# Optimization experiments

Hardware: AMD Instinct MI355X
Metric: run time of the kernel (lower is better)

## Reference

```python
import jax, jax.numpy as jnp
import numpy as np

N, E, T, D, A = 16384, 65536, 2048, 64, 6


def _w(k, shape, fan_in):
    return jax.random.normal(k, shape, jnp.float32) / np.sqrt(fan_in)


def setup_inputs() -> dict:
    key = jax.random.key(0)
    ks = jax.random.split(key, 20)
    inp = {}
    inp["x"] = jax.random.normal(ks[0], (N, 3), jnp.float32)
    inp["edge_attr"] = jax.random.normal(ks[1], (E, 7), jnp.float32)
    inp["edge_index"] = jax.random.randint(ks[2], (2, E), 0, N)
    inp["nonring"] = jax.random.randint(ks[3], (T, 4), 0, N)
    inp["hx"] = jnp.zeros((1, D), jnp.float32)
    inp["cx"] = jnp.zeros((1, D), jnp.float32)
    inp["W_lin0"] = _w(ks[4], (D, 3), 3); inp["b_lin0"] = jnp.zeros((D,), jnp.float32)
    inp["W_e1"] = _w(ks[5], (128, 7), 7); inp["b_e1"] = jnp.zeros((128,), jnp.float32)
    inp["W_e2"] = _w(ks[6], (D * D, 128), 128); inp["b_e2"] = jnp.zeros((D * D,), jnp.float32)
    inp["conv_root"] = _w(ks[7], (D, D), D); inp["conv_bias"] = jnp.zeros((D,), jnp.float32)
    inp["gru_Wih"] = _w(ks[8], (3 * D, D), D); inp["gru_Whh"] = _w(ks[9], (3 * D, D), D)
    inp["gru_bih"] = jnp.zeros((3 * D,), jnp.float32); inp["gru_bhh"] = jnp.zeros((3 * D,), jnp.float32)
    inp["s2s_Wih"] = _w(ks[10], (4 * D, 2 * D), 2 * D); inp["s2s_Whh"] = _w(ks[11], (4 * D, D), D)
    inp["s2s_bih"] = jnp.zeros((4 * D,), jnp.float32); inp["s2s_bhh"] = jnp.zeros((4 * D,), jnp.float32)
    inp["mem_Wih"] = _w(ks[12], (4 * D, 2 * D), 2 * D); inp["mem_Whh"] = _w(ks[13], (4 * D, D), D)
    inp["mem_bih"] = jnp.zeros((4 * D,), jnp.float32); inp["mem_bhh"] = jnp.zeros((4 * D,), jnp.float32)
    inp["W_lin1"] = _w(ks[14], (D, 5 * D), 5 * D); inp["b_lin1"] = jnp.zeros((D,), jnp.float32)
    inp["W_lin2"] = _w(ks[15], (A, D), D); inp["b_lin2"] = jnp.zeros((A,), jnp.float32)
    inp["W_lin3"] = _w(ks[16], (1, 3 * D), 3 * D); inp["b_lin3"] = jnp.zeros((1,), jnp.float32)
    return inp


def _lstm_cell(xin, h, c, Wih, Whh, bih, bhh):
    g = xin @ Wih.T + bih + h @ Whh.T + bhh
    i, f, gg, o = jnp.split(g, 4, axis=-1)  # torch gate order i,f,g,o
    c = jax.nn.sigmoid(f) * c + jax.nn.sigmoid(i) * jnp.tanh(gg)
    h = jax.nn.sigmoid(o) * jnp.tanh(c)
    return h, c


def _gru_cell(xin, h, Wih, Whh, bih, bhh):
    gi = xin @ Wih.T + bih
    gh = h @ Whh.T + bhh
    ir, iz, inn = jnp.split(gi, 3, axis=-1)  # torch gate order r,z,n
    hr, hz, hn = jnp.split(gh, 3, axis=-1)
    r = jax.nn.sigmoid(ir + hr)
    z = jax.nn.sigmoid(iz + hz)
    n = jnp.tanh(inn + r * hn)
    return (1.0 - z) * n + z * h


def reference(x, edge_attr, edge_index, nonring, hx, cx,
              W_lin0, b_lin0, W_e1, b_e1, W_e2, b_e2, conv_root, conv_bias,
              gru_Wih, gru_Whh, gru_bih, gru_bhh,
              s2s_Wih, s2s_Whh, s2s_bih, s2s_bhh,
              mem_Wih, mem_Whh, mem_bih, mem_bhh,
              W_lin1, b_lin1, W_lin2, b_lin2, W_lin3, b_lin3):
    src, tgt = edge_index[0], edge_index[1]
    out = jax.nn.relu(x @ W_lin0.T + b_lin0)  # [N, D]
    h = out  # GRU hidden (nodes as batch)
    # edge-conditioned dim x dim matrices (NNConv edge MLP)
    ew = jax.nn.relu(edge_attr @ W_e1.T + b_e1)
    ew = (ew @ W_e2.T + b_e2).reshape(E, D, D)  # [E, D, D]
    cnt = jnp.maximum(jax.ops.segment_sum(jnp.ones((E,), out.dtype), tgt, num_segments=N), 1.0)
    for _ in range(3):
        msg = jnp.einsum('ed,edf->ef', out[src], ew)  # per-edge small matmul
        aggr = jax.ops.segment_sum(msg, tgt, num_segments=N) / cnt[:, None]  # scatter-mean
        m = jax.nn.relu(aggr + out @ conv_root + conv_bias)  # NNConv root + bias, then relu
        h = _gru_cell(m, h, gru_Wih, gru_Whh, gru_bih, gru_bhh)
        out = h
    # Set2Set pooling (single graph, B=1), processing_steps=3
    hs = jnp.zeros((1, D), out.dtype)
    cs = jnp.zeros((1, D), out.dtype)
    q_star = jnp.zeros((1, 2 * D), out.dtype)
    for _ in range(3):
        hs, cs = _lstm_cell(q_star, hs, cs, s2s_Wih, s2s_Whh, s2s_bih, s2s_bhh)
        a = jax.nn.softmax(out @ hs[0])  # [N]
        r = (a[:, None] * out).sum(0, keepdims=True)  # [1, D]
        q_star = jnp.concatenate([hs, r], axis=1)
    pool = q_star  # [1, 2D]
    lstm_out, cx_new = _lstm_cell(pool, hx, cx, mem_Wih, mem_Whh, mem_bih, mem_bhh)
    hx_new = lstm_out
    # torsion head: index_select -> view(4*D, -1) -> permute(1,0)
    sel = out[nonring.reshape(-1)]  # [4T, D]
    tfeat = sel.reshape(4 * D, -1).T  # [T, 4D], faithful to torch view semantics
    rep = jnp.repeat(lstm_out.reshape(-1), T).reshape(T, D)  # torch repeat_interleave + view
    pf = jnp.concatenate([tfeat, rep], axis=1)  # [T, 5D]
    logits = jax.nn.relu(pf @ W_lin1.T + b_lin1) @ W_lin2.T + b_lin2  # [T, A]
    v = jnp.concatenate([pool, lstm_out], axis=1) @ W_lin3.T + b_lin3  # [1, 1]
    return logits, v, hx_new, cx_new
```

## Files before the change

kernel.cpp:

```cpp
#include <hip/hip_runtime.h>

#define cN 16384
#define cE 65536
#define cT 2048
#define CAP 88

typedef __attribute__((ext_vector_type(8))) short short8;
typedef __attribute__((ext_vector_type(4))) float f32x4;
typedef __attribute__((ext_vector_type(4))) unsigned u32x4;

__device__ __forceinline__ short f2bf(float f){
  unsigned u = __float_as_uint(f);
  u = (u + 0x7FFFu + ((u >> 16) & 1u)) >> 16;
  return (short)u;
}
__device__ __forceinline__ float bf2f(short s){
  return __uint_as_float(((unsigned)(unsigned short)s) << 16);
}
__device__ __forceinline__ unsigned cvtpk(float lo, float hi){
  unsigned r;
  asm("v_cvt_pk_bf16_f32 %0, %1, %2" : "=v"(r) : "v"(lo), "v"(hi));
  return r;
}
__device__ __forceinline__ float sigm(float x){ return 1.f / (1.f + __expf(-x)); }
__device__ __forceinline__ float wred(float v){
  v += __shfl_xor(v, 32); v += __shfl_xor(v, 16); v += __shfl_xor(v, 8);
  v += __shfl_xor(v, 4);  v += __shfl_xor(v, 2);  v += __shfl_xor(v, 1);
  return v;
}
__device__ __forceinline__ float wredmax(float v){
  v = fmaxf(v, __shfl_xor(v, 32)); v = fmaxf(v, __shfl_xor(v, 16));
  v = fmaxf(v, __shfl_xor(v, 8));  v = fmaxf(v, __shfl_xor(v, 4));
  v = fmaxf(v, __shfl_xor(v, 2));  v = fmaxf(v, __shfl_xor(v, 1));
  return v;
}

#define B_L0   4096
#define B_H1   20480
#define B_W2   22528
#define B_B2   22544
#define B_WP   22656
#define B_DEG  22912
__global__ __launch_bounds__(256) void k_setup(
    const float* __restrict__ x, const float* __restrict__ Wl0, const float* __restrict__ bl0,
    float* __restrict__ out,
    const float* __restrict__ ea, const float* __restrict__ We1, const float* __restrict__ be1,
    unsigned* __restrict__ h1p,
    const float* __restrict__ W2, short* __restrict__ w2f,
    const float* __restrict__ b2, short* __restrict__ b2f,
    const float* __restrict__ convW, const float* __restrict__ gWih,
    const float* __restrict__ gWhh, short* __restrict__ wpk,
    const int* __restrict__ ei, int* __restrict__ deg)
{
  int b = blockIdx.x, tid = threadIdx.x;
  if (b < B_L0){
    int i = b * 256 + tid;
    int n = i >> 6, f = i & 63;
    float acc = bl0[f] + x[n*3]*Wl0[f*3] + x[n*3+1]*Wl0[f*3+1] + x[n*3+2]*Wl0[f*3+2];
    out[i] = fmaxf(acc, 0.f);
  } else if (b < B_H1){
    int i = (b - B_L0) * 256 + tid;
    int e = i >> 6, k = i & 63;
    const float* a  = ea + e * 7;
    const float* w0 = We1 + k * 7;
    const float* w1 = We1 + (k + 64) * 7;
    float a0 = be1[k], a1 = be1[k + 64];
    #pragma unroll
    for (int c = 0; c < 7; c++){ float av = a[c]; a0 += av * w0[c]; a1 += av * w1[c]; }
    unsigned lo = (unsigned short)f2bf(fmaxf(a0, 0.f));
    unsigned hi = (unsigned short)f2bf(fmaxf(a1, 0.f));
    h1p[i] = lo | (hi << 16);
  } else if (b < B_W2){
    int o = (b - B_H1) * 256 + tid;
    int j = o & 7, l = (o >> 3) & 63, ks = (o >> 9) & 31, c = (o >> 14) & 7, fb = (o >> 17) & 3;
    int f = fb * 16 + (l & 15);
    int d = c * 8 + j;
    int k = ks * 4 + ((l >> 4) & 3);
    w2f[o] = f2bf(W2[(d * 64 + f) * 128 + k]);
  } else if (b < B_B2){
    int o = (b - B_W2) * 256 + tid;
    int j = o & 7, l = (o >> 3) & 63, ks2 = (o >> 9) & 1, fb = (o >> 10) & 3;
    int d = ks2 * 32 + ((l >> 4) & 3) * 8 + j;
    int f = fb * 16 + (l & 15);
    b2f[o] = f2bf(b2[d * 64 + f]);
  } else if (b < B_WP){
    int o = (b - B_B2) * 256 + tid;
    int j = o & 7, l = (o >> 3) & 63, kc = (o >> 9) & 1, cb = o >> 10;
    int k = kc * 32 + ((l >> 4) & 3) * 8 + j;
    int c16 = l & 15;
    float v;
    if (cb < 4)       v = convW[k * 64 + cb * 16 + c16];
    else if (cb < 16) v = gWih[((cb - 4) * 16 + c16) * 64 + k];
    else              v = gWhh[((cb - 16) * 16 + c16) * 64 + k];
    wpk[o] = f2bf(v);
  } else {
    int e = (b - B_WP) * 256 + tid;
    atomicAdd(&deg[ei[cE + e]], 1);
  }
}

__global__ __launch_bounds__(1024) void k_scan(const int* __restrict__ deg,
    int* __restrict__ rowp, int* __restrict__ cur, float* __restrict__ cnt)
{
  __shared__ int part[1024];
  int tid = threadIdx.x;
  int base = tid * 16;
  int loc[16]; int s = 0;
  #pragma unroll
  for (int i = 0; i < 16; i++){ loc[i] = s; s += deg[base + i]; }
  part[tid] = s;
  __syncthreads();
  for (int off = 1; off < 1024; off <<= 1){
    int v = (tid >= off) ? part[tid - off] : 0;
    __syncthreads();
    part[tid] += v;
    __syncthreads();
  }
  int inc = part[tid];
  int eb = inc - s;
  #pragma unroll
  for (int i = 0; i < 16; i++){
    int rv = eb + loc[i];
    rowp[base + i] = rv;
    cur[base + i] = rv;
    int dv = deg[base + i];
    cnt[base + i] = (float)(dv > 0 ? dv : 1);
  }
  if (tid == 1023) rowp[16384] = inc;
}

__global__ __launch_bounds__(256) void k_scatter(const int* __restrict__ ei,
    int* __restrict__ cur, int* __restrict__ esrc, int* __restrict__ eidx)
{
  int e = blockIdx.x * 256 + threadIdx.x;
  int t = ei[cE + e];
  int pos = atomicAdd(&cur[t], 1);
  esrc[pos] = ei[e];
  eidx[pos] = e;
}

__global__ __launch_bounds__(256, 2) void k_sagg(const float* __restrict__ outR,
    float* __restrict__ outW,
    const unsigned* __restrict__ h1p, const short* __restrict__ w2f,
    const short* __restrict__ b2f, const short* __restrict__ wpk,
    const float* __restrict__ convB, const float* __restrict__ bih,
    const float* __restrict__ bhh, const float* __restrict__ cnt,
    const int* __restrict__ rowp, const int* __restrict__ esrc,
    const int* __restrict__ eidx)
{
  __shared__ __align__(16) short S[16][1040];
  __shared__ __align__(16) unsigned h1i[CAP][64];
  __shared__ __align__(16) float outsf[CAP][64];
  __shared__ __align__(16) short osb[16][72];
  int tid = threadIdx.x, w = tid >> 6, lane = tid & 63;
  int t0 = blockIdx.x * 16;

  int ebase = rowp[t0];
  int eend  = rowp[t0 + 16];
  int ecnt  = eend - ebase;
  bool fits = (ecnt <= CAP);
  int scnt  = fits ? ecnt : CAP;
  for (int i = w; i < scnt; i += 4){
    int eid = eidx[ebase + i];
    int src = esrc[ebase + i];
    h1i[i][lane] = h1p[(size_t)eid * 64 + lane];
    outsf[i][lane] = outR[(size_t)src * 64 + lane];
  }
  int toff[4], tcnt[4];
  #pragma unroll
  for (int g = 0; g < 4; g++){
    int t = t0 + w * 4 + g;
    int a = rowp[t], b = rowp[t + 1];
    toff[g] = a - ebase; tcnt[g] = b - a;
  }
  short8 breg[32];
  {
    const short* bb0 = w2f + ((size_t)(w * 8) * 32) * 512 + lane * 8;
    #pragma unroll
    for (int ks = 0; ks < 32; ++ks)
      breg[ks] = *(const short8*)(bb0 + (size_t)ks * 512);
  }
  __syncthreads();

  #pragma unroll
  for (int g = 0; g < 4; g++){
    int ti = w * 4 + g;
    float os = 0.f;
    int tf = toff[g], tc = tcnt[g];
    for (int p = 0; p < tc; p++){
      int slot = tf + p;
      if (slot < CAP) os += outsf[slot][lane];
      else            os += outR[(size_t)esrc[ebase + slot] * 64 + lane];
    }
    osb[ti][lane] = (short)cvtpk(os, os);
  }

  f32x4 acc[4] = {{0,0,0,0},{0,0,0,0},{0,0,0,0},{0,0,0,0}};
  int arow = lane & 15, kg = lane >> 4;
  for (int c = 0; c < 8; ++c){
    #pragma unroll
    for (int g = 0; g < 4; ++g){
      int ti = w * 4 + g;
      float a0[8], a1[8];
      #pragma unroll
      for (int d = 0; d < 8; d++){ a0[d] = 0.f; a1[d] = 0.f; }
      int tc = tcnt[g], tf = toff[g];
      if (fits){
        #pragma unroll 2
        for (int p = 0; p < tc; ++p){
          int slot = tf + p;
          unsigned u = h1i[slot][lane];
          float h1a = __uint_as_float(u << 16);
          float h1b = __uint_as_float(u & 0xFFFF0000u);
          f32x4 o0 = *(const f32x4*)&outsf[slot][c * 8];
          f32x4 o1 = *(const f32x4*)&outsf[slot][c * 8 + 4];
          a0[0] = fmaf(o0[0], h1a, a0[0]); a1[0] = fmaf(o0[0], h1b, a1[0]);
          a0[1] = fmaf(o0[1], h1a, a0[1]); a1[1] = fmaf(o0[1], h1b, a1[1]);
          a0[2] = fmaf(o0[2], h1a, a0[2]); a1[2] = fmaf(o0[2], h1b, a1[2]);
          a0[3] = fmaf(o0[3], h1a, a0[3]); a1[3] = fmaf(o0[3], h1b, a1[3]);
          a0[4] = fmaf(o1[0], h1a, a0[4]); a1[4] = fmaf(o1[0], h1b, a1[4]);
          a0[5] = fmaf(o1[1], h1a, a0[5]); a1[5] = fmaf(o1[1], h1b, a1[5]);
          a0[6] = fmaf(o1[2], h1a, a0[6]); a1[6] = fmaf(o1[2], h1b, a1[6]);
          a0[7] = fmaf(o1[3], h1a, a0[7]); a1[7] = fmaf(o1[3], h1b, a1[7]);
        }
      } else {
        for (int p = 0; p < tc; ++p){
          int slot = tf + p;
          if (slot < CAP){
            unsigned u = h1i[slot][lane];
            float h1a = __uint_as_float(u << 16);
            float h1b = __uint_as_float(u & 0xFFFF0000u);
            f32x4 o0 = *(const f32x4*)&outsf[slot][c * 8];
            f32x4 o1 = *(const f32x4*)&outsf[slot][c * 8 + 4];
            #pragma unroll
            for (int d = 0; d < 4; d++){
              a0[d] = fmaf(o0[d], h1a, a0[d]); a1[d] = fmaf(o0[d], h1b, a1[d]);
              a0[4+d] = fmaf(o1[d], h1a, a0[4+d]); a1[4+d] = fmaf(o1[d], h1b, a1[4+d]);
            }
          } else {
            int eid = eidx[ebase + slot];
            int src = esrc[ebase + slot];
            unsigned u = h1p[(size_t)eid * 64 + lane];
            float h1a = __uint_as_float(u << 16);
            float h1b = __uint_as_float(u & 0xFFFF0000u);
            #pragma unroll
            for (int d = 0; d < 8; d++){
              float o = outR[(size_t)src * 64 + c * 8 + d];
              a0[d] = fmaf(o, h1a, a0[d]); a1[d] = fmaf(o, h1b, a1[d]);
            }
          }
        }
      }
      u32x4 p0, p1;
      p0[0] = cvtpk(a0[0], a0[1]); p0[1] = cvtpk(a0[2], a0[3]);
      p0[2] = cvtpk(a0[4], a0[5]); p0[3] = cvtpk(a0[6], a0[7]);
      p1[0] = cvtpk(a1[0], a1[1]); p1[1] = cvtpk(a1[2], a1[3]);
      p1[2] = cvtpk(a1[4], a1[5]); p1[3] = cvtpk(a1[6], a1[7]);
      *(u32x4*)&S[ti][lane * 8]       = p0;
      *(u32x4*)&S[ti][512 + lane * 8] = p1;
    }
    __syncthreads();
    const short* bbn = w2f + ((size_t)(w * 8 + c + 1) * 32) * 512 + lane * 8;
    bool more = (c < 7);
    #pragma unroll
    for (int ks8 = 0; ks8 < 8; ++ks8){
      #pragma unroll
      for (int j = 0; j < 4; ++j){
        int ks = ks8 * 4 + j;
        short8 afr = *(const short8*)&S[arow][ks * 32 + kg * 8];
        acc[j] = __builtin_amdgcn_mfma_f32_16x16x32_bf16(afr, breg[ks], acc[j], 0, 0, 0);
        if (more) breg[ks] = *(const short8*)(bbn + (size_t)ks * 512);
      }
    }
    __syncthreads();
  }
  #pragma unroll
  for (int ks2 = 0; ks2 < 2; ++ks2){
    short8 osf = *(const short8*)&osb[arow][ks2 * 32 + kg * 8];
    short8 bfr = *(const short8*)(b2f + ((size_t)((w * 2 + ks2) * 64 + lane)) * 8);
    acc[ks2] = __builtin_amdgcn_mfma_f32_16x16x32_bf16(osf, bfr, acc[ks2], 0, 0, 0);
  }
  f32x4 accT;
  #pragma unroll
  for (int q = 0; q < 4; q++)
    accT[q] = (acc[0][q] + acc[1][q]) + (acc[2][q] + acc[3][q]);

  int fcol = w * 16 + arow;
  int trow = kg * 4;
  short* tA  = (short*)&h1i[0][0];
  short* mAp = tA + 16 * 72;
  for (int i = tid; i < 512; i += 256){
    int r = i >> 5, c2 = (i & 31) * 2;
    float2 v = *(const float2*)&outR[(size_t)(t0 + r) * 64 + c2];
    *(unsigned*)&tA[r * 72 + c2] = cvtpk(v.x, v.y);
  }
  __syncthreads();
  const short8* WF = (const short8*)wpk;
  short8 aof0 = *(const short8*)&tA[arow * 72 + kg * 8];
  short8 aof1 = *(const short8*)&tA[arow * 72 + 32 + kg * 8];
  f32x4 cz = {0.f, 0.f, 0.f, 0.f};
  f32x4 cva0 = __builtin_amdgcn_mfma_f32_16x16x32_bf16(aof0, WF[(w * 2 + 0) * 64 + lane], cz, 0, 0, 0);
  f32x4 cva1 = __builtin_amdgcn_mfma_f32_16x16x32_bf16(aof1, WF[(w * 2 + 1) * 64 + lane], cz, 0, 0, 0);
  float cb_ = convB[fcol];
  #pragma unroll
  for (int q = 0; q < 4; q++){
    int node = t0 + trow + q;
    float icq = 1.0f / fmaxf(cnt[node], 1.0f);
    float m = fmaxf(accT[q] * icq + cva0[q] + cva1[q] + cb_, 0.f);
    mAp[(trow + q) * 72 + fcol] = f2bf(m);
  }
  __syncthreads();
  short8 amf0 = *(const short8*)&mAp[arow * 72 + kg * 8];
  short8 amf1 = *(const short8*)&mAp[arow * 72 + 32 + kg * 8];
  f32x4 gir = {0,0,0,0}, giz = {0,0,0,0}, gin = {0,0,0,0};
  f32x4 ghr = {0,0,0,0}, ghz = {0,0,0,0}, ghn = {0,0,0,0};
  gir = __builtin_amdgcn_mfma_f32_16x16x32_bf16(amf0, WF[((4  + w) * 2 + 0) * 64 + lane], gir, 0, 0, 0);
  gir = __builtin_amdgcn_mfma_f32_16x16x32_bf16(amf1, WF[((4  + w) * 2 + 1) * 64 + lane], gir, 0, 0, 0);
  giz = __builtin_amdgcn_mfma_f32_16x16x32_bf16(amf0, WF[((8  + w) * 2 + 0) * 64 + lane], giz, 0, 0, 0);
  giz = __builtin_amdgcn_mfma_f32_16x16x32_bf16(amf1, WF[((8  + w) * 2 + 1) * 64 + lane], giz, 0, 0, 0);
  gin = __builtin_amdgcn_mfma_f32_16x16x32_bf16(amf0, WF[((12 + w) * 2 + 0) * 64 + lane], gin, 0, 0, 0);
  gin = __builtin_amdgcn_mfma_f32_16x16x32_bf16(amf1, WF[((12 + w) * 2 + 1) * 64 + lane], gin, 0, 0, 0);
  ghr = __builtin_amdgcn_mfma_f32_16x16x32_bf16(aof0, WF[((16 + w) * 2 + 0) * 64 + lane], ghr, 0, 0, 0);
  ghr = __builtin_amdgcn_mfma_f32_16x16x32_bf16(aof1, WF[((16 + w) * 2 + 1) * 64 + lane], ghr, 0, 0, 0);
  ghz = __builtin_amdgcn_mfma_f32_16x16x32_bf16(aof0, WF[((20 + w) * 2 + 0) * 64 + lane], ghz, 0, 0, 0);
  ghz = __builtin_amdgcn_mfma_f32_16x16x32_bf16(aof1, WF[((20 + w) * 2 + 1) * 64 + lane], ghz, 0, 0, 0);
  ghn = __builtin_amdgcn_mfma_f32_16x16x32_bf16(aof0, WF[((24 + w) * 2 + 0) * 64 + lane], ghn, 0, 0, 0);
  ghn = __builtin_amdgcn_mfma_f32_16x16x32_bf16(aof1, WF[((24 + w) * 2 + 1) * 64 + lane], ghn, 0, 0, 0);
  float bir = bih[fcol], biz = bih[64 + fcol], bin_ = bih[128 + fcol];
  float bhr = bhh[fcol], bhz = bhh[64 + fcol], bhn = bhh[128 + fcol];
  #pragma unroll
  for (int q = 0; q < 4; q++){
    size_t node = (size_t)(t0 + trow + q);
    float rr = sigm(gir[q] + bir + ghr[q] + bhr);
    float zz = sigm(giz[q] + biz + ghz[q] + bhz);
    float nn = tanhf(gin[q] + bin_ + rr * (ghn[q] + bhn));
    float o = outR[node * 64 + fcol];
    outW[node * 64 + fcol] = (1.f - zz) * nn + zz * o;
  }
}

__global__ __launch_bounds__(256) void k_dotsF(const float* __restrict__ out,
    const float* __restrict__ Wih, const float* __restrict__ Whh,
    const float* __restrict__ bih, const float* __restrict__ bhh,
    float* __restrict__ scal,
    const float* __restrict__ rbI, const float* __restrict__ bmI, const float* __restrict__ esI,
    float* __restrict__ rbO, float* __restrict__ bmO, float* __restrict__ esO, int st)
{
  __shared__ float q[128];
  __shared__ float hsL[64];
  __shared__ float gsh[4][64];
  __shared__ float hsh[64];
  __shared__ float smax[4];
  __shared__ float otile[64][64];
  __shared__ float sarr[64];
  __shared__ float ebuf[64];
  __shared__ float rpart[4][64];
  __shared__ float redA[4], redB[4];
  const float* pg = scal + st * 256;
  float* pn = scal + (st + 1) * 256;
  int tid = threadIdx.x, gg = tid >> 6, lane = tid & 63;
  if (st > 0){
    float bm = bmI[tid];
    float m = wredmax(bm);
    if (lane == 0) redA[gg] = m;
    __syncthreads();
    float gmax = fmaxf(fmaxf(redA[0], redA[1]), fmaxf(redA[2], redA[3]));
    float ep = wred(__expf(bm - gmax) * esI[tid]);
    if (lane == 0) redB[gg] = ep;
    float racc = 0.f;
    for (int i = 0; i < 64; i++){
      int b = gg * 64 + i;
      racc += __expf(bmI[b] - gmax) * rbI[b * 64 + lane];
    }
    rpart[gg][lane] = racc;
    __syncthreads();
    if (gg == 0){
      float esum = redB[0] + redB[1] + redB[2] + redB[3];
      float r = rpart[0][lane] + rpart[1][lane] + rpart[2][lane] + rpart[3][lane];
      q[64 + lane] = r / esum;
    }
  } else if (gg == 0) q[64 + lane] = 0.f;
  if (gg == 0){
    float hs = (st == 0) ? 0.f : pg[lane];
    q[lane] = hs; hsL[lane] = hs;
  }
  __syncthreads();
  float2 fq = *(const float2*)&q[2 * lane];
  float hv0 = hsL[lane];
  #pragma unroll 4
  for (int o = 0; o < 64; o++){
    int row = gg * 64 + o;
    float2 wv = *(const float2*)&Wih[(size_t)row * 128 + 2 * lane];
    float s = wv.x * fq.x + wv.y * fq.y + Whh[(size_t)row * 64 + lane] * hv0;
    s = wred(s);
    if (lane == 0) gsh[gg][o] = s;
  }
  __syncthreads();
  if (gg == 0){
    float gi = gsh[0][lane] + bih[lane]       + bhh[lane];
    float gf = gsh[1][lane] + bih[64 + lane]  + bhh[64 + lane];
    float gv = gsh[2][lane] + bih[128 + lane] + bhh[128 + lane];
    float go = gsh[3][lane] + bih[192 + lane] + bhh[192 + lane];
    float cs = (st == 0) ? 0.f : pg[64 + lane];
    float cn = sigm(gf) * cs + sigm(gi) * tanhf(gv);
    float hn = sigm(go) * tanhf(cn);
    hsh[lane] = hn;
    if (blockIdx.x == 0){ pn[lane] = hn; pn[64 + lane] = cn; }
  }
  __syncthreads();
  int nbase = blockIdx.x * 64 + gg * 16;
  float hv = hsh[lane];
  float wmax = -3.4e38f;
  #pragma unroll 4
  for (int i = 0; i < 16; i++){
    float v = out[(size_t)(nbase + i) * 64 + lane];
    otile[gg * 16 + i][lane] = v;
    float p = wred(v * hv);
    if (lane == 0) sarr[gg * 16 + i] = p;
    wmax = fmaxf(wmax, p);
  }
  if (lane == 0) smax[gg] = wmax;
  __syncthreads();
  float bm = fmaxf(fmaxf(smax[0], smax[1]), fmaxf(smax[2], smax[3]));
  if (tid < 64) ebuf[tid] = __expf(sarr[tid] - bm);
  __syncthreads();
  float racc = 0.f;
  #pragma unroll 4
  for (int i = 0; i < 16; i++)
    racc += ebuf[gg * 16 + i] * otile[gg * 16 + i][lane];
  rpart[gg][lane] = racc;
  __syncthreads();
  if (gg == 0){
    float r = rpart[0][lane] + rpart[1][lane] + rpart[2][lane] + rpart[3][lane];
    rbO[blockIdx.x * 64 + lane] = r;
  } else if (gg == 1){
    float es = wred(ebuf[lane]);
    if (lane == 0) esO[blockIdx.x] = es;
  } else if (gg == 2 && lane == 0) bmO[blockIdx.x] = bm;
}

__global__ __launch_bounds__(256) void k_smFin(
    const float* __restrict__ rbI, const float* __restrict__ bmI, const float* __restrict__ esI,
    const float* __restrict__ Wih, const float* __restrict__ Whh,
    const float* __restrict__ bih, const float* __restrict__ bhh,
    const float* __restrict__ hx, const float* __restrict__ cx,
    const float* __restrict__ W3, const float* __restrict__ b3,
    float* __restrict__ scal, float* __restrict__ dout)
{
  __shared__ float redA[4], redB[4];
  __shared__ float rpart[4][64];
  __shared__ float pool[128];
  __shared__ float hxs[64];
  __shared__ float gsh[4][64];
  __shared__ float lob[64];
  int tid = threadIdx.x, wid = tid >> 6, lane = tid & 63;
  float bm = bmI[tid];
  float m = wredmax(bm);
  if (lane == 0) redA[wid] = m;
  __syncthreads();
  float gmax = fmaxf(fmaxf(redA[0], redA[1]), fmaxf(redA[2], redA[3]));
  float ep = wred(__expf(bm - gmax) * esI[tid]);
  if (lane == 0) redB[wid] = ep;
  float racc = 0.f;
  for (int i = 0; i < 64; i++){
    int b = wid * 64 + i;
    racc += __expf(bmI[b] - gmax) * rbI[b * 64 + lane];
  }
  rpart[wid][lane] = racc;
  __syncthreads();
  if (wid == 0){
    float esum = redB[0] + redB[1] + redB[2] + redB[3];
    float r = rpart[0][lane] + rpart[1][lane] + rpart[2][lane] + rpart[3][lane];
    pool[lane] = scal[3 * 256 + lane];
    pool[64 + lane] = r / esum;
    hxs[lane] = hx[lane];
  }
  __syncthreads();
  float2 fq = *(const float2*)&pool[2 * lane];
  float hv = hxs[lane];
  #pragma unroll 4
  for (int o = 0; o < 64; o++){
    int row = wid * 64 + o;
    float2 wv = *(const float2*)&Wih[(size_t)row * 128 + 2 * lane];
    float s = wv.x * fq.x + wv.y * fq.y + Whh[(size_t)row * 64 + lane] * hv;
    s = wred(s);
    if (lane == 0) gsh[wid][o] = s;
  }
  __syncthreads();
  if (wid == 0){
    float gi = gsh[0][lane] + bih[lane]       + bhh[lane];
    float gf = gsh[1][lane] + bih[64 + lane]  + bhh[64 + lane];
    float gv = gsh[2][lane] + bih[128 + lane] + bhh[128 + lane];
    float go = gsh[3][lane] + bih[192 + lane] + bhh[192 + lane];
    float cn = sigm(gf) * cx[lane] + sigm(gi) * tanhf(gv);
    float hn = sigm(go) * tanhf(cn);
    dout[12289 + lane] = hn;
    dout[12353 + lane] = cn;
    scal[1024 + lane] = hn;
    lob[lane] = hn;
  }
  __syncthreads();
  if (wid == 0){
    float a = pool[lane] * W3[lane] + pool[64 + lane] * W3[64 + lane]
            + lob[lane] * W3[128 + lane];
    a = wred(a);
    if (lane == 0) dout[12288] = a + b3[0];
  }
}

__global__ __launch_bounds__(256) void k_head(const float* __restrict__ out,
    const int* __restrict__ nr, const float* __restrict__ scal,
    const float* __restrict__ W1, const float* __restrict__ b1,
    const float* __restrict__ W2, const float* __restrict__ b2,
    float* __restrict__ dout)
{
  __shared__ float pf[4][320];
  __shared__ float hb[4][64];
  int tid = threadIdx.x, wid = tid >> 6, lane = tid & 63;
  int t = blockIdx.x * 4 + wid;
  float lo = scal[1024 + (t >> 5)];
  #pragma unroll
  for (int rep = 0; rep < 4; rep++){
    int j = rep * 64 + lane;
    int idx = nr[j * 32 + (t >> 6)];
    pf[wid][j] = out[idx * 64 + (t & 63)];
  }
  pf[wid][256 + lane] = lo;
  __syncthreads();
  float acc = b1[lane];
  const float* w = W1 + lane * 320;
  #pragma unroll 4
  for (int j = 0; j < 320; j++) acc += pf[wid][j] * w[j];
  hb[wid][lane] = fmaxf(acc, 0.f);
  __syncthreads();
  if (lane < 6){
    float a2 = b2[lane];
    const float* w2 = W2 + lane * 64;
    #pragma unroll 4
    for (int f = 0; f < 64; f++) a2 += hb[wid][f] * w2[f];
    dout[t * 6 + lane] = a2;
  }
}

extern "C" void kernel_launch(void* const* d_in, const int* in_sizes, int n_in,
                              void* d_out, int out_size, void* d_ws, size_t ws_size,
                              hipStream_t stream)
{
  const float* x         = (const float*)d_in[0];
  const float* edge_attr = (const float*)d_in[1];
  const int*   ei        = (const int*)d_in[2];
  const int*   nonring   = (const int*)d_in[3];
  const float* hx        = (const float*)d_in[4];
  const float* cx        = (const float*)d_in[5];
  const float* W_lin0 = (const float*)d_in[6];  const float* b_lin0 = (const float*)d_in[7];
  const float* W_e1   = (const float*)d_in[8];  const float* b_e1   = (const float*)d_in[9];
  const float* W_e2   = (const float*)d_in[10]; const float* b_e2   = (const float*)d_in[11];
  const float* convW  = (const float*)d_in[12]; const float* convB  = (const float*)d_in[13];
  const float* gWih   = (const float*)d_in[14]; const float* gWhh   = (const float*)d_in[15];
  const float* gbih   = (const float*)d_in[16]; const float* gbhh   = (const float*)d_in[17];
  const float* sWih   = (const float*)d_in[18]; const float* sWhh   = (const float*)d_in[19];
  const float* sbih   = (const float*)d_in[20]; const float* sbhh   = (const float*)d_in[21];
  const float* mWih   = (const float*)d_in[22]; const float* mWhh   = (const float*)d_in[23];
  const float* mbih   = (const float*)d_in[24]; const float* mbhh   = (const float*)d_in[25];
  const float* W_lin1 = (const float*)d_in[26]; const float* b_lin1 = (const float*)d_in[27];
  const float* W_lin2 = (const float*)d_in[28]; const float* b_lin2 = (const float*)d_in[29];
  const float* W_lin3 = (const float*)d_in[30]; const float* b_lin3 = (const float*)d_in[31];
  float* dout = (float*)d_out;

  char* w = (char*)d_ws;
  float* outb = (float*)w;  w += (size_t)cN * 64 * 4;
  float* outb2= (float*)w;  w += (size_t)cN * 64 * 4;
  unsigned* h1p = (unsigned*)w;  w += (size_t)cE * 64 * 4;
  short* w2f  = (short*)w;  w += (size_t)64 * 8192 * 2;
  short* b2f  = (short*)w;  w += 4096 * 2;
  short* wpk  = (short*)w;  w += 28672 * 2;
  float* cntb = (float*)w;  w += cN * 4;
  float* rbufA= (float*)w;  w += 256 * 64 * 4;
  float* rbufB= (float*)w;  w += 256 * 64 * 4;
  float* bmA  = (float*)w;  w += 256 * 4;
  float* bmB  = (float*)w;  w += 256 * 4;
  float* esA  = (float*)w;  w += 256 * 4;
  float* esB  = (float*)w;  w += 256 * 4;
  float* scal = (float*)w;  w += 1088 * 4;
  int* deg  = (int*)w;  w += cN * 4;
  int* cur  = (int*)w;  w += cN * 4;
  int* rowp = (int*)w;  w += (cN + 1) * 4 + 60;
  int* esrc = (int*)w;  w += cE * 4;
  int* eidx = (int*)w;  w += cE * 4;

  hipMemsetAsync(deg, 0, cN * 4, stream);

  k_setup<<<B_DEG, 256, 0, stream>>>(x, W_lin0, b_lin0, outb,
      edge_attr, W_e1, b_e1, h1p, W_e2, w2f, b_e2, b2f,
      convW, gWih, gWhh, wpk, ei, deg);
  k_scan<<<1, 1024, 0, stream>>>(deg, rowp, cur, cntb);
  k_scatter<<<cE / 256, 256, 0, stream>>>(ei, cur, esrc, eidx);

  k_sagg<<<cN / 16, 256, 0, stream>>>(outb,  outb2, h1p, w2f, b2f, wpk, convB,
      gbih, gbhh, cntb, rowp, esrc, eidx);
  k_sagg<<<cN / 16, 256, 0, stream>>>(outb2, outb,  h1p, w2f, b2f, wpk, convB,
      gbih, gbhh, cntb, rowp, esrc, eidx);
  k_sagg<<<cN / 16, 256, 0, stream>>>(outb,  outb2, h1p, w2f, b2f, wpk, convB,
      gbih, gbhh, cntb, rowp, esrc, eidx);

  k_dotsF<<<cN / 64, 256, 0, stream>>>(outb2, sWih, sWhh, sbih, sbhh, scal,
      rbufA, bmA, esA, rbufA, bmA, esA, 0);
  k_dotsF<<<cN / 64, 256, 0, stream>>>(outb2, sWih, sWhh, sbih, sbhh, scal,
      rbufA, bmA, esA, rbufB, bmB, esB, 1);
  k_dotsF<<<cN / 64, 256, 0, stream>>>(outb2, sWih, sWhh, sbih, sbhh, scal,
      rbufB, bmB, esB, rbufA, bmA, esA, 2);
  k_smFin<<<1, 256, 0, stream>>>(rbufA, bmA, esA,
      mWih, mWhh, mbih, mbhh, hx, cx, W_lin3, b_lin3, scal, dout);

  k_head<<<cT / 4, 256, 0, stream>>>(outb2, nonring, scal, W_lin1, b_lin1, W_lin2, b_lin2, dout);
}
```

Measured before the change: 499.6 us.

## Balance per-wave edge work by degree-sorted target assignment; drop B-fragment register prefetch

Result: faster. 484.0 us (-3.1%).

```diff
diff --git a/kernel.cpp b/kernel.cpp
--- a/kernel.cpp
+++ b/kernel.cpp
@@ -139,7 +139,7 @@
   eidx[pos] = e;
 }
 
-__global__ __launch_bounds__(256, 2) void k_sagg(const float* __restrict__ outR,
+__global__ __launch_bounds__(256) void k_sagg(const float* __restrict__ outR,
     float* __restrict__ outW,
     const unsigned* __restrict__ h1p, const short* __restrict__ w2f,
     const short* __restrict__ b2f, const short* __restrict__ wpk,
@@ -152,6 +152,7 @@
   __shared__ __align__(16) unsigned h1i[CAP][64];
   __shared__ __align__(16) float outsf[CAP][64];
   __shared__ __align__(16) short osb[16][72];
+  __shared__ int ordb[32];
   int tid = threadIdx.x, w = tid >> 6, lane = tid & 63;
   int t0 = blockIdx.x * 16;
 
@@ -166,25 +167,33 @@
     h1i[i][lane] = h1p[(size_t)eid * 64 + lane];
     outsf[i][lane] = outR[(size_t)src * 64 + lane];
   }
-  int toff[4], tcnt[4];
+  if (tid < 16) ordb[tid] = rowp[t0 + tid + 1] - rowp[t0 + tid];
+  __syncthreads();
+  if (tid < 16){
+    int d = ordb[tid];
+    int rank = 0;
+    #pragma unroll
+    for (int j = 0; j < 16; j++){
+      int dj = ordb[j];
+      rank += (dj > d) || (dj == d && j < tid);
+    }
+    ordb[16 + rank] = tid;
+  }
+  __syncthreads();
+  int tsel[4], toff[4], tcnt[4];
   #pragma unroll
   for (int g = 0; g < 4; g++){
-    int t = t0 + w * 4 + g;
+    int pos = g * 4 + ((g & 1) ? (3 - w) : w);
+    int ti = ordb[16 + pos];
+    tsel[g] = ti;
+    int t = t0 + ti;
     int a = rowp[t], b = rowp[t + 1];
     toff[g] = a - ebase; tcnt[g] = b - a;
   }
-  short8 breg[32];
-  {
-    const short* bb0 = w2f + ((size_t)(w * 8) * 32) * 512 + lane * 8;
-    #pragma unroll
-    for (int ks = 0; ks < 32; ++ks)
-      breg[ks] = *(const short8*)(bb0 + (size_t)ks * 512);
-  }
-  __syncthreads();
 
   #pragma unroll
   for (int g = 0; g < 4; g++){
-    int ti = w * 4 + g;
+    int ti = tsel[g];
     float os = 0.f;
     int tf = toff[g], tc = tcnt[g];
     for (int p = 0; p < tc; p++){
@@ -200,7 +209,7 @@
   for (int c = 0; c < 8; ++c){
     #pragma unroll
     for (int g = 0; g < 4; ++g){
-      int ti = w * 4 + g;
+      int ti = tsel[g];
       float a0[8], a1[8];
       #pragma unroll
       for (int d = 0; d < 8; d++){ a0[d] = 0.f; a1[d] = 0.f; }
@@ -260,16 +269,15 @@
       *(u32x4*)&S[ti][512 + lane * 8] = p1;
     }
     __syncthreads();
-    const short* bbn = w2f + ((size_t)(w * 8 + c + 1) * 32) * 512 + lane * 8;
-    bool more = (c < 7);
+    const short* bbase = w2f + ((size_t)(w * 8 + c) * 32) * 512 + lane * 8;
     #pragma unroll
     for (int ks8 = 0; ks8 < 8; ++ks8){
       #pragma unroll
       for (int j = 0; j < 4; ++j){
         int ks = ks8 * 4 + j;
         short8 afr = *(const short8*)&S[arow][ks * 32 + kg * 8];
-        acc[j] = __builtin_amdgcn_mfma_f32_16x16x32_bf16(afr, breg[ks], acc[j], 0, 0, 0);
-        if (more) breg[ks] = *(const short8*)(bbn + (size_t)ks * 512);
+        short8 bfr = *(const short8*)(bbase + (size_t)ks * 512);
+        acc[j] = __builtin_amdgcn_mfma_f32_16x16x32_bf16(afr, bfr, acc[j], 0, 0, 0);
       }
     }
     __syncthreads();
```
